# Kernel optimization log

Hardware: AMD Instinct MI355X
Metric: run time of the kernel (lower is better)

The kernel has to match this reference:

```python
import jax, jax.numpy as jnp
import numpy as np

B, T, E = 4, 2048, 1024
H, D = 16, 64  # num_heads, head_size; H*D == E


def setup_inputs() -> dict:
    key = jax.random.key(0)
    ks = jax.random.split(key, 8)
    s = 0.02
    x = jax.random.normal(ks[0], (B, T, E), dtype=jnp.float32)
    attention_mask = jnp.ones((B, T), dtype=jnp.float32)
    # stacked per-head projection weights (no bias), torch Linear: y = x @ W.T
    Wq = jax.random.normal(ks[1], (H, E, D), dtype=jnp.float32) * s
    Wk = jax.random.normal(ks[2], (H, E, D), dtype=jnp.float32) * s
    Wv = jax.random.normal(ks[3], (H, E, D), dtype=jnp.float32) * s
    Wo = jax.random.normal(ks[4], (E, E), dtype=jnp.float32) * s
    bo = jnp.zeros((E,), dtype=jnp.float32)
    return {"x": x, "attention_mask": attention_mask, "Wq": Wq, "Wk": Wk,
            "Wv": Wv, "Wo": Wo, "bo": bo}


def reference(x, attention_mask, Wq, Wk, Wv, Wo, bo):
    # per-head projections, vectorized over heads: [B,T,E] x [H,E,D] -> [B,H,T,D]
    q = jnp.einsum('bte,hed->bhtd', x, Wq)
    k = jnp.einsum('bte,hed->bhtd', x, Wk)
    v = jnp.einsum('bte,hed->bhtd', x, Wv)
    scores = jnp.einsum('bhtd,bhsd->bhts', q, k) / jnp.sqrt(jnp.float32(D))
    # causal mask (tril): masked_fill with -inf
    causal = jnp.tril(jnp.ones((T, T), dtype=bool))
    scores = jnp.where(causal[None, None, :, :], scores, -jnp.inf)
    # padding mask: weights += (1 - mask) * finfo(float32).min, broadcast over queries
    neg = jnp.finfo(jnp.float32).min
    scores = scores + ((1.0 - attention_mask) * neg)[:, None, None, :]
    weights = jax.nn.softmax(scores, axis=-1)
    out = jnp.einsum('bhts,bhsd->bthd', weights, v).reshape(B, T, H * D)
    return out @ Wo.T + bo
```

## Files before the change

kernel.cpp:

```cpp
#include <hip/hip_runtime.h>
#include <hip/hip_bf16.h>

#define B_ 4
#define T_ 2048
#define E_ 1024
#define H_ 16
#define D_ 64
#define M_ (B_*T_)

typedef short bf16x8 __attribute__((ext_vector_type(8)));
typedef float f32x4  __attribute__((ext_vector_type(4)));
typedef float f32x16 __attribute__((ext_vector_type(16)));

__device__ __forceinline__ short f2bf(float f) {
    __hip_bfloat16 h = __float2bfloat16(f);
    return *reinterpret_cast<short*>(&h);
}

__device__ __forceinline__ unsigned int pk2(float a, float b) {
    unsigned int ua = __float_as_uint(a), ub = __float_as_uint(b);
    return ((ua + 0x8000u) >> 16) | ((ub + 0x8000u) & 0xffff0000u);
}

__device__ __forceinline__ void async_ld16(const void* g, void* l) {
    __builtin_amdgcn_global_load_lds(
        (const __attribute__((address_space(1))) unsigned int*)g,
        (__attribute__((address_space(3))) unsigned int*)l, 16, 0, 0);
}

__global__ void conv_bf16(const float* __restrict__ src, short* __restrict__ dst) {
    const int i = blockIdx.x * 256 + threadIdx.x;
    float4 v = ((const float4*)src)[i];
    short4 o = make_short4(f2bf(v.x), f2bf(v.y), f2bf(v.z), f2bf(v.w));
    ((short4*)dst)[i] = o;
}

__global__ void bias_prep(const float* __restrict__ mask, float* __restrict__ bias) {
    const int i = blockIdx.x * 256 + threadIdx.x;
    float bm = (1.0f - mask[i]) * -3.402823466e38f;
    bias[i] = fmaf(bm, 1.4426950f, -8.6561700f);
}

__global__ void wtrans(const float* __restrict__ Wq,
                       const float* __restrict__ Wk,
                       const float* __restrict__ Wv,
                       short* __restrict__ Wt) {
    const int which = blockIdx.z;
    const float* __restrict__ W = (which == 0) ? Wq : (which == 1) ? Wk : Wv;
    const int h  = blockIdx.y;
    const int e0 = blockIdx.x * 64;

    __shared__ float tile[64][65];
    const int tid = threadIdx.x;

#pragma unroll
    for (int r = 0; r < 4; ++r) {
        int lin = tid + r * 256;
        int er = lin >> 4, c4 = (lin & 15) * 4;
        float4 v = *(const float4*)(W + ((size_t)h * E_ + e0 + er) * D_ + c4);
        tile[er][c4 + 0] = v.x; tile[er][c4 + 1] = v.y;
        tile[er][c4 + 2] = v.z; tile[er][c4 + 3] = v.w;
    }
    __syncthreads();
#pragma unroll
    for (int r = 0; r < 4; ++r) {
        int lin = tid + r * 256;
        int dr = lin >> 4, j4 = (lin & 15) * 4;
        short4 o = make_short4(f2bf(tile[j4 + 0][dr]), f2bf(tile[j4 + 1][dr]),
                               f2bf(tile[j4 + 2][dr]), f2bf(tile[j4 + 3][dr]));
        *(short4*)(Wt + ((size_t)which * 1024 + h * 64 + dr) * E_ + e0 + j4) = o;
    }
}

template <int MODE>
__global__ __launch_bounds__(256) void mfma_gemm(
        const short* __restrict__ A,
        const short* __restrict__ Bt,
        short* __restrict__ qo, short* __restrict__ ko, short* __restrict__ vo,
        float* __restrict__ Cout, const float* __restrict__ bo) {
    __shared__ __align__(16) short As[128 * 32];
    __shared__ __align__(16) short Bs[128 * 32];

    const int tid  = threadIdx.x;
    const int wave = tid >> 6, lane = tid & 63;
    const int c = lane & 15, quad = lane >> 4;
    const int wm = wave >> 1, wn = wave & 1;
    const int m0 = blockIdx.x * 128;
    const int n0 = blockIdx.y * 128;

    int rowS[2], kgS[2];
#pragma unroll
    for (int r = 0; r < 2; ++r) {
        int p = r * 256 + wave * 64 + lane;
        rowS[r] = p >> 2;
        kgS[r]  = (p & 3) ^ ((rowS[r] >> 1) & 3);
    }

    f32x4 acc[4][4] = {};

    for (int k0 = 0; k0 < 1024; k0 += 32) {
#pragma unroll
        for (int r = 0; r < 2; ++r) {
            async_ld16(A  + (size_t)(m0 + rowS[r]) * 1024 + k0 + kgS[r] * 8,
                       As + (r * 256 + wave * 64) * 8);
            async_ld16(Bt + (size_t)(n0 + rowS[r]) * 1024 + k0 + kgS[r] * 8,
                       Bs + (r * 256 + wave * 64) * 8);
        }
        __syncthreads();

        bf16x8 af[4], bf[4];
#pragma unroll
        for (int mi = 0; mi < 4; ++mi) {
            int row = wm * 64 + mi * 16 + c;
            int pos = row * 4 + (quad ^ ((row >> 1) & 3));
            af[mi] = *(const bf16x8*)(As + pos * 8);
        }
#pragma unroll
        for (int ni = 0; ni < 4; ++ni) {
            int row = wn * 64 + ni * 16 + c;
            int pos = row * 4 + (quad ^ ((row >> 1) & 3));
            bf[ni] = *(const bf16x8*)(Bs + pos * 8);
        }
#pragma unroll
        for (int mi = 0; mi < 4; ++mi)
#pragma unroll
            for (int ni = 0; ni < 4; ++ni)
                acc[mi][ni] = __builtin_amdgcn_mfma_f32_16x16x32_bf16(
                    af[mi], bf[ni], acc[mi][ni], 0, 0, 0);
        __syncthreads();
    }

    if (MODE == 0) {
        const int which = n0 >> 10;
        const int nb = n0 & 1023;
        if (which == 2) {
#pragma unroll
            for (int mi = 0; mi < 4; ++mi) {
                const int m = m0 + wm * 64 + mi * 16 + quad * 4;
                const int b = m >> 11, t = m & 2047;
#pragma unroll
                for (int ni = 0; ni < 4; ++ni) {
                    const int n = nb + wn * 64 + ni * 16 + c;
                    const int h = n >> 6, d = n & 63;
                    short4 s4 = make_short4(f2bf(acc[mi][ni][0]), f2bf(acc[mi][ni][1]),
                                            f2bf(acc[mi][ni][2]), f2bf(acc[mi][ni][3]));
                    *(short4*)(vo + (((size_t)b * H_ + h) * D_ + d) * T_ + t) = s4;
                }
            }
        } else {
            short* __restrict__ outp = (which == 0) ? qo : ko;
#pragma unroll
            for (int mi = 0; mi < 4; ++mi) {
#pragma unroll
                for (int i = 0; i < 4; ++i) {
                    const int m = m0 + wm * 64 + mi * 16 + quad * 4 + i;
                    const int b = m >> 11, t = m & 2047;
#pragma unroll
                    for (int ni = 0; ni < 4; ++ni) {
                        const int n = nb + wn * 64 + ni * 16 + c;
                        const int h = n >> 6, d = n & 63;
                        outp[(((size_t)b * H_ + h) * T_ + t) * D_ + d] =
                            f2bf(acc[mi][ni][i]);
                    }
                }
            }
        }
    } else {
#pragma unroll
        for (int mi = 0; mi < 4; ++mi) {
#pragma unroll
            for (int i = 0; i < 4; ++i) {
                const int m = m0 + wm * 64 + mi * 16 + quad * 4 + i;
#pragma unroll
                for (int ni = 0; ni < 4; ++ni) {
                    const int n = n0 + wn * 64 + ni * 16 + c;
                    Cout[(size_t)m * E_ + n] = acc[mi][ni][i] + bo[n];
                }
            }
        }
    }
}

__global__ __launch_bounds__(256) void flash_attn4(
        const short* __restrict__ qg,
        const short* __restrict__ kg,
        const short* __restrict__ vtg,
        const float* __restrict__ biasg,
        short* __restrict__ attn) {
    const int h = blockIdx.x, b = blockIdx.y;
    const int kblk = 15 - blockIdx.z;
    const int Q0 = kblk * 128;
    const int tid  = threadIdx.x;
    const int wave = tid >> 6, lane = tid & 63;
    const int ln = lane & 31, hi = lane >> 5;
    const int strip = 4 * kblk + wave;
    const int q0w = Q0 + wave * 32;
    const int nt = 4 * kblk + 4;

    __shared__ __align__(16) char lds[16384];

    const size_t bh = (size_t)b * H_ + h;
    const short* qbh  = qg  + bh * (size_t)T_ * D_;
    const short* kbh  = kg  + bh * (size_t)T_ * D_;
    const short* vtbh = vtg + bh * (size_t)D_ * T_;
    const float* biasb = biasg + (size_t)b * T_;

    const int ks = tid >> 3, kgs = (tid & 7) ^ (ks & 7);
    const int vd = tid >> 2, vgs = (tid & 3) ^ (vd & 3);

    int kaddr[4];
#pragma unroll
    for (int kc = 0; kc < 4; ++kc)
        kaddr[kc] = ln * 128 + ((((kc << 1) + hi) ^ (ln & 7)) << 4);
    int vaddr[4];
#pragma unroll
    for (int dh = 0; dh < 2; ++dh)
#pragma unroll
        for (int kc2 = 0; kc2 < 2; ++kc2) {
            int d = dh * 32 + ln;
            vaddr[dh * 2 + kc2] =
                4096 + d * 64 + ((((kc2 << 1) + hi) ^ (d & 3)) << 4);
        }

    bf16x8 qf[4];
#pragma unroll
    for (int kc = 0; kc < 4; ++kc)
        qf[kc] = *(const bf16x8*)(qbh + (size_t)(q0w + ln) * D_ + kc * 16 + hi * 8);

    f32x16 O0 = {}, O1 = {};
    float lacc = 0.0f;

#define STAGE_T(s0v, boff) do {                                             \
        async_ld16(kbh + (size_t)((s0v) + ks) * D_ + (kgs << 3),            \
                   lds + (boff) + wave * 1024);                             \
        async_ld16(vtbh + (size_t)vd * T_ + (s0v) + (vgs << 3),             \
                   lds + (boff) + 4096 + wave * 1024);                      \
    } while (0)

    STAGE_T(0, 0);
    __syncthreads();

    int bufoff = 0;
    for (int tt = 0; tt < nt; ++tt) {
        if (tt + 1 < nt) STAGE_T((tt + 1) << 5, bufoff ^ 8192);

        if (tt <= strip) {
            const int s0 = tt << 5;

            float4 b4[4];
#pragma unroll
            for (int g = 0; g < 4; ++g)
                b4[g] = *(const float4*)(biasb + s0 + g * 8 + hi * 4);

            f32x16 S = {};
#pragma unroll
            for (int kc = 0; kc < 4; ++kc) {
                bf16x8 ka = *(const bf16x8*)(lds + bufoff + kaddr[kc]);
                S = __builtin_amdgcn_mfma_f32_32x32x16_bf16(ka, qf[kc], S, 0, 0, 0);
            }

            float p[16];
#pragma unroll
            for (int r = 0; r < 16; ++r) {
                float bb = ((const float*)&b4[r >> 2])[r & 3];
                p[r] = __builtin_amdgcn_exp2f(fmaf(S[r], 0.18033688f, bb));
            }
            if (tt == strip) {
#pragma unroll
                for (int r = 0; r < 16; ++r)
                    if (((r & 3) + ((r >> 2) << 3) + (hi << 2)) > ln)
                        p[r] = 0.0f;
            }
            {
                float t0 = (p[0] + p[1]) + (p[2] + p[3]);
                float t1 = (p[4] + p[5]) + (p[6] + p[7]);
                float t2 = (p[8] + p[9]) + (p[10] + p[11]);
                float t3 = (p[12] + p[13]) + (p[14] + p[15]);
                lacc += (t0 + t1) + (t2 + t3);
            }

            unsigned int u0 = pk2(p[0], p[1]),  u1 = pk2(p[2], p[3]);
            unsigned int u2 = pk2(p[4], p[5]),  u3 = pk2(p[6], p[7]);
            unsigned int u4 = pk2(p[8], p[9]),  u5 = pk2(p[10], p[11]);
            unsigned int u6 = pk2(p[12], p[13]), u7 = pk2(p[14], p[15]);
            asm("v_permlane32_swap_b32 %0, %1" : "+v"(u0), "+v"(u2));
            asm("v_permlane32_swap_b32 %0, %1" : "+v"(u1), "+v"(u3));
            asm("v_permlane32_swap_b32 %0, %1" : "+v"(u4), "+v"(u6));
            asm("v_permlane32_swap_b32 %0, %1" : "+v"(u5), "+v"(u7));
            union { unsigned int w[4]; bf16x8 v; } pa0, pa1;
            pa0.w[0] = u0; pa0.w[1] = u1; pa0.w[2] = u2; pa0.w[3] = u3;
            pa1.w[0] = u4; pa1.w[1] = u5; pa1.w[2] = u6; pa1.w[3] = u7;

            {
                bf16x8 v00 = *(const bf16x8*)(lds + bufoff + vaddr[0]);
                bf16x8 v01 = *(const bf16x8*)(lds + bufoff + vaddr[1]);
                O0 = __builtin_amdgcn_mfma_f32_32x32x16_bf16(pa0.v, v00, O0, 0, 0, 0);
                O0 = __builtin_amdgcn_mfma_f32_32x32x16_bf16(pa1.v, v01, O0, 0, 0, 0);
                bf16x8 v10 = *(const bf16x8*)(lds + bufoff + vaddr[2]);
                bf16x8 v11 = *(const bf16x8*)(lds + bufoff + vaddr[3]);
                O1 = __builtin_amdgcn_mfma_f32_32x32x16_bf16(pa0.v, v10, O1, 0, 0, 0);
                O1 = __builtin_amdgcn_mfma_f32_32x32x16_bf16(pa1.v, v11, O1, 0, 0, 0);
            }
        }

        __syncthreads();
        bufoff ^= 8192;
    }
#undef STAGE_T

    unsigned int la = __float_as_uint(lacc), lb2 = la;
    asm("v_permlane32_swap_b32 %0, %1" : "+v"(la), "+v"(lb2));
    const float ltot = __uint_as_float(la) + __uint_as_float(lb2);

    float* lsh = (float*)lds + wave * 32;
    if (hi == 0) lsh[ln] = 1.0f / ltot;
    __syncthreads();

    short* ab = attn + (size_t)b * T_ * E_ + h * D_;
#pragma unroll
    for (int r = 0; r < 16; ++r) {
        const int qrow = (r & 3) + ((r >> 2) << 3) + (hi << 2);
        const float iv = lsh[qrow];
        const size_t base = (size_t)(q0w + qrow) * E_;
        ab[base + ln]      = f2bf(O0[r] * iv);
        ab[base + 32 + ln] = f2bf(O1[r] * iv);
    }
}

extern "C" void kernel_launch(void* const* d_in, const int* in_sizes, int n_in,
                              void* d_out, int out_size, void* d_ws, size_t ws_size,
                              hipStream_t stream) {
    const float* x    = (const float*)d_in[0];
    const float* mask = (const float*)d_in[1];
    const float* Wq   = (const float*)d_in[2];
    const float* Wk   = (const float*)d_in[3];
    const float* Wv   = (const float*)d_in[4];
    const float* Wo   = (const float*)d_in[5];
    const float* bo   = (const float*)d_in[6];
    float* out        = (float*)d_out;

    const size_t S = (size_t)M_ * E_;
    char* ws = (char*)d_ws;
    short* xb   = (short*)ws;
    short* qb   = (short*)(ws + S * 2);
    short* kb   = (short*)(ws + S * 4);
    short* vtb  = (short*)(ws + S * 6);
    short* Wt   = (short*)(ws + S * 8);
    short* Wob  = (short*)(ws + S * 8 + (size_t)3 * 1024 * 1024 * 2);
    float* bias = (float*)(ws + S * 8 + (size_t)4 * 1024 * 1024 * 2);
    short* attnb = xb;

    conv_bf16<<<dim3(M_ * E_ / 1024), 256, 0, stream>>>(x, xb);
    conv_bf16<<<dim3(E_ * E_ / 1024), 256, 0, stream>>>(Wo, Wob);
    wtrans<<<dim3(E_ / 64, H_, 3), 256, 0, stream>>>(Wq, Wk, Wv, Wt);
    bias_prep<<<dim3(B_ * T_ / 256), 256, 0, stream>>>(mask, bias);

    mfma_gemm<0><<<dim3(M_ / 128, 3 * E_ / 128), 256, 0, stream>>>(
        xb, Wt, qb, kb, vtb, nullptr, nullptr);

    flash_attn4<<<dim3(H_, B_, 16), 256, 0, stream>>>(qb, kb, vtb, bias, attnb);

    mfma_gemm<1><<<dim3(M_ / 128, E_ / 128), 256, 0, stream>>>(
        attnb, Wob, nullptr, nullptr, nullptr, out, bo);
}
```

Baseline: 275.9 us.

## Pair causal query blocks per workgroup and stage bias in LDS

The attention grid is halved, and each workgroup now handles two query blocks (15-z and z) in sequence. Every workgroup then does the same amount of causal work instead of the heavily imbalanced per-block load. The softmax scale is folded into Q in the projection epilogue, and the key-padding bias row is async-loaded once into LDS rather than read from global memory each tile. The V swizzle changes from XOR to an additive rotation, and __syncthreads is replaced with explicit vmcnt waits plus s_barrier so the next tile's loads can stay in flight. The cost is less grid parallelism (512 workgroups), more LDS per block, and bf16 rounding applied to the pre-scaled Q.

```diff
diff --git a/kernel.cpp b/kernel.cpp
--- a/kernel.cpp
+++ b/kernel.cpp
@@ -149,6 +149,7 @@
             }
         } else {
             short* __restrict__ outp = (which == 0) ? qo : ko;
+            const float sc = (which == 0) ? 0.18033688f : 1.0f;
 #pragma unroll
             for (int mi = 0; mi < 4; ++mi) {
 #pragma unroll
@@ -160,7 +161,7 @@
                         const int n = nb + wn * 64 + ni * 16 + c;
                         const int h = n >> 6, d = n & 63;
                         outp[(((size_t)b * H_ + h) * T_ + t) * D_ + d] =
-                            f2bf(acc[mi][ni][i]);
+                            f2bf(acc[mi][ni][i] * sc);
                     }
                 }
             }
@@ -181,23 +182,19 @@
     }
 }
 
-__global__ __launch_bounds__(256) void flash_attn4(
+__global__ __launch_bounds__(256) void flash_attn5(
         const short* __restrict__ qg,
         const short* __restrict__ kg,
         const short* __restrict__ vtg,
         const float* __restrict__ biasg,
         short* __restrict__ attn) {
     const int h = blockIdx.x, b = blockIdx.y;
-    const int kblk = 15 - blockIdx.z;
-    const int Q0 = kblk * 128;
+    const int z = blockIdx.z;
     const int tid  = threadIdx.x;
     const int wave = tid >> 6, lane = tid & 63;
     const int ln = lane & 31, hi = lane >> 5;
-    const int strip = 4 * kblk + wave;
-    const int q0w = Q0 + wave * 32;
-    const int nt = 4 * kblk + 4;
-
-    __shared__ __align__(16) char lds[16384];
+
+    __shared__ __align__(16) char lds[25088];
 
     const size_t bh = (size_t)b * H_ + h;
     const short* qbh  = qg  + bh * (size_t)T_ * D_;
@@ -206,7 +203,7 @@
     const float* biasb = biasg + (size_t)b * T_;
 
     const int ks = tid >> 3, kgs = (tid & 7) ^ (ks & 7);
-    const int vd = tid >> 2, vgs = (tid & 3) ^ (vd & 3);
+    const int vd = tid >> 2, vgs = ((tid & 3) - ((tid >> 3) & 3)) & 3;
 
     int kaddr[4];
 #pragma unroll
@@ -219,16 +216,13 @@
         for (int kc2 = 0; kc2 < 2; ++kc2) {
             int d = dh * 32 + ln;
             vaddr[dh * 2 + kc2] =
-                4096 + d * 64 + ((((kc2 << 1) + hi) ^ (d & 3)) << 4);
-        }
-
-    bf16x8 qf[4];
-#pragma unroll
-    for (int kc = 0; kc < 4; ++kc)
-        qf[kc] = *(const bf16x8*)(qbh + (size_t)(q0w + ln) * D_ + kc * 16 + hi * 8);
-
-    f32x16 O0 = {}, O1 = {};
-    float lacc = 0.0f;
+                4096 + d * 64 + (((((kc2 << 1) + hi) + (d >> 1)) & 3) << 4);
+        }
+
+#pragma unroll
+    for (int r = 0; r < 2; ++r)
+        async_ld16(biasb + 4 * (r * 256 + wave * 64 + lane),
+                   lds + 16384 + r * 4096 + wave * 1024);
 
 #define STAGE_T(s0v, boff) do {                                             \
         async_ld16(kbh + (size_t)((s0v) + ks) * D_ + (kgs << 3),            \
@@ -237,61 +231,79 @@
                    lds + (boff) + 4096 + wave * 1024);                      \
     } while (0)
 
-    STAGE_T(0, 0);
-    __syncthreads();
-
-    int bufoff = 0;
-    for (int tt = 0; tt < nt; ++tt) {
-        if (tt + 1 < nt) STAGE_T((tt + 1) << 5, bufoff ^ 8192);
-
-        if (tt <= strip) {
-            const int s0 = tt << 5;
-
-            float4 b4[4];
-#pragma unroll
-            for (int g = 0; g < 4; ++g)
-                b4[g] = *(const float4*)(biasb + s0 + g * 8 + hi * 4);
-
-            f32x16 S = {};
-#pragma unroll
-            for (int kc = 0; kc < 4; ++kc) {
-                bf16x8 ka = *(const bf16x8*)(lds + bufoff + kaddr[kc]);
-                S = __builtin_amdgcn_mfma_f32_32x32x16_bf16(ka, qf[kc], S, 0, 0, 0);
-            }
-
-            float p[16];
-#pragma unroll
-            for (int r = 0; r < 16; ++r) {
-                float bb = ((const float*)&b4[r >> 2])[r & 3];
-                p[r] = __builtin_amdgcn_exp2f(fmaf(S[r], 0.18033688f, bb));
-            }
-            if (tt == strip) {
-#pragma unroll
-                for (int r = 0; r < 16; ++r)
-                    if (((r & 3) + ((r >> 2) << 3) + (hi << 2)) > ln)
-                        p[r] = 0.0f;
-            }
-            {
-                float t0 = (p[0] + p[1]) + (p[2] + p[3]);
-                float t1 = (p[4] + p[5]) + (p[6] + p[7]);
-                float t2 = (p[8] + p[9]) + (p[10] + p[11]);
-                float t3 = (p[12] + p[13]) + (p[14] + p[15]);
-                lacc += (t0 + t1) + (t2 + t3);
-            }
-
-            unsigned int u0 = pk2(p[0], p[1]),  u1 = pk2(p[2], p[3]);
-            unsigned int u2 = pk2(p[4], p[5]),  u3 = pk2(p[6], p[7]);
-            unsigned int u4 = pk2(p[8], p[9]),  u5 = pk2(p[10], p[11]);
-            unsigned int u6 = pk2(p[12], p[13]), u7 = pk2(p[14], p[15]);
-            asm("v_permlane32_swap_b32 %0, %1" : "+v"(u0), "+v"(u2));
-            asm("v_permlane32_swap_b32 %0, %1" : "+v"(u1), "+v"(u3));
-            asm("v_permlane32_swap_b32 %0, %1" : "+v"(u4), "+v"(u6));
-            asm("v_permlane32_swap_b32 %0, %1" : "+v"(u5), "+v"(u7));
-            union { unsigned int w[4]; bf16x8 v; } pa0, pa1;
-            pa0.w[0] = u0; pa0.w[1] = u1; pa0.w[2] = u2; pa0.w[3] = u3;
-            pa1.w[0] = u4; pa1.w[1] = u5; pa1.w[2] = u6; pa1.w[3] = u7;
-
-            {
+#pragma unroll 1
+    for (int sidx = 0; sidx < 2; ++sidx) {
+        const int kblk = sidx ? z : (15 - z);
+        const int q0w = kblk * 128 + wave * 32;
+        const int mytile = 4 * kblk + wave;
+        const int nt = 4 * kblk + 4;
+
+        bf16x8 qf[4];
+#pragma unroll
+        for (int kc = 0; kc < 4; ++kc)
+            qf[kc] = *(const bf16x8*)(qbh + (size_t)(q0w + ln) * D_ + kc * 16 + hi * 8);
+
+        f32x16 O0 = {}, O1 = {};
+        float lacc = 0.0f;
+
+        STAGE_T(0, 0);
+        int bufoff = 0;
+        for (int tt = 0; tt < nt; ++tt) {
+            if (tt + 1 < nt) {
+                STAGE_T((tt + 1) << 5, bufoff ^ 8192);
+                asm volatile("s_waitcnt vmcnt(2)" ::: "memory");
+            } else {
+                asm volatile("s_waitcnt vmcnt(0)" ::: "memory");
+            }
+            __builtin_amdgcn_s_barrier();
+
+            if (tt <= mytile) {
+                const int s0 = tt << 5;
+
+                f32x4 b4[4];
+#pragma unroll
+                for (int g = 0; g < 4; ++g)
+                    b4[g] = *(const f32x4*)(lds + 16384 + (s0 + g * 8 + hi * 4) * 4);
+
+                f32x16 S = {};
+#pragma unroll
+                for (int kc = 0; kc < 4; ++kc) {
+                    bf16x8 ka = *(const bf16x8*)(lds + bufoff + kaddr[kc]);
+                    S = __builtin_amdgcn_mfma_f32_32x32x16_bf16(ka, qf[kc], S, 0, 0, 0);
+                }
+
+                float p[16];
+#pragma unroll
+                for (int r = 0; r < 16; ++r) {
+                    float bb = ((const float*)&b4[r >> 2])[r & 3];
+                    p[r] = __builtin_amdgcn_exp2f(S[r] + bb);
+                }
+                if (tt == mytile) {
+#pragma unroll
+                    for (int r = 0; r < 16; ++r)
+                        if (((r & 3) + ((r >> 2) << 3) + (hi << 2)) > ln)
+                            p[r] = 0.0f;
+                }
+                {
+                    float t0 = (p[0] + p[1]) + (p[2] + p[3]);
+                    float t1 = (p[4] + p[5]) + (p[6] + p[7]);
+                    float t2 = (p[8] + p[9]) + (p[10] + p[11]);
+                    float t3 = (p[12] + p[13]) + (p[14] + p[15]);
+                    lacc += (t0 + t1) + (t2 + t3);
+                }
+
+                unsigned int u0 = pk2(p[0], p[1]),  u1 = pk2(p[2], p[3]);
+                unsigned int u2 = pk2(p[4], p[5]),  u3 = pk2(p[6], p[7]);
+                unsigned int u4 = pk2(p[8], p[9]),  u5 = pk2(p[10], p[11]);
+                unsigned int u6 = pk2(p[12], p[13]), u7 = pk2(p[14], p[15]);
+                asm("v_permlane32_swap_b32 %0, %1" : "+v"(u0), "+v"(u2));
+                asm("v_permlane32_swap_b32 %0, %1" : "+v"(u1), "+v"(u3));
+                asm("v_permlane32_swap_b32 %0, %1" : "+v"(u4), "+v"(u6));
+                asm("v_permlane32_swap_b32 %0, %1" : "+v"(u5), "+v"(u7));
+                union { unsigned int w[4]; bf16x8 v; } pa0, pa1;
+                pa0.w[0] = u0; pa0.w[1] = u1; pa0.w[2] = u2; pa0.w[3] = u3;
+                pa1.w[0] = u4; pa1.w[1] = u5; pa1.w[2] = u6; pa1.w[3] = u7;
+
                 bf16x8 v00 = *(const bf16x8*)(lds + bufoff + vaddr[0]);
                 bf16x8 v01 = *(const bf16x8*)(lds + bufoff + vaddr[1]);
                 O0 = __builtin_amdgcn_mfma_f32_32x32x16_bf16(pa0.v, v00, O0, 0, 0, 0);
@@ -301,30 +313,30 @@
                 O1 = __builtin_amdgcn_mfma_f32_32x32x16_bf16(pa0.v, v10, O1, 0, 0, 0);
                 O1 = __builtin_amdgcn_mfma_f32_32x32x16_bf16(pa1.v, v11, O1, 0, 0, 0);
             }
-        }
-
+
+            __builtin_amdgcn_s_barrier();
+            bufoff ^= 8192;
+        }
+
+        unsigned int la = __float_as_uint(lacc), lb2 = la;
+        asm("v_permlane32_swap_b32 %0, %1" : "+v"(la), "+v"(lb2));
+        const float ltot = __uint_as_float(la) + __uint_as_float(lb2);
+
+        float* lsh = (float*)(lds + 24576) + wave * 32;
+        if (hi == 0) lsh[ln] = 1.0f / ltot;
         __syncthreads();
-        bufoff ^= 8192;
+
+        short* ab = attn + (size_t)b * T_ * E_ + h * D_;
+#pragma unroll
+        for (int r = 0; r < 16; ++r) {
+            const int qrow = (r & 3) + ((r >> 2) << 3) + (hi << 2);
+            const float iv = lsh[qrow];
+            const size_t base = (size_t)(q0w + qrow) * E_;
+            ab[base + ln]      = f2bf(O0[r] * iv);
+            ab[base + 32 + ln] = f2bf(O1[r] * iv);
+        }
     }
 #undef STAGE_T
-
-    unsigned int la = __float_as_uint(lacc), lb2 = la;
-    asm("v_permlane32_swap_b32 %0, %1" : "+v"(la), "+v"(lb2));
-    const float ltot = __uint_as_float(la) + __uint_as_float(lb2);
-
-    float* lsh = (float*)lds + wave * 32;
-    if (hi == 0) lsh[ln] = 1.0f / ltot;
-    __syncthreads();
-
-    short* ab = attn + (size_t)b * T_ * E_ + h * D_;
-#pragma unroll
-    for (int r = 0; r < 16; ++r) {
-        const int qrow = (r & 3) + ((r >> 2) << 3) + (hi << 2);
-        const float iv = lsh[qrow];
-        const size_t base = (size_t)(q0w + qrow) * E_;
-        ab[base + ln]      = f2bf(O0[r] * iv);
-        ab[base + 32 + ln] = f2bf(O1[r] * iv);
-    }
 }
 
 extern "C" void kernel_launch(void* const* d_in, const int* in_sizes, int n_in,
@@ -358,7 +370,7 @@
     mfma_gemm<0><<<dim3(M_ / 128, 3 * E_ / 128), 256, 0, stream>>>(
         xb, Wt, qb, kb, vtb, nullptr, nullptr);
 
-    flash_attn4<<<dim3(H_, B_, 16), 256, 0, stream>>>(qb, kb, vtb, bias, attnb);
+    flash_attn5<<<dim3(H_, B_, 8), 256, 0, stream>>>(qb, kb, vtb, bias, attnb);
 
     mfma_gemm<1><<<dim3(M_ / 128, E_ / 128), 256, 0, stream>>>(
         attnb, Wob, nullptr, nullptr, nullptr, out, bo);
```

Measured after the change: 270.1 us. 1.02x faster.
